# Optimization experiments

Hardware: AMD Instinct MI355X
Metric: run time of the kernel (lower is better)

## Reference

```python
import jax, jax.numpy as jnp
import numpy as np

INPUT = 28
STEPS = 28
HIDDEN = 128
LABELS = 10
FORGET_BIAS = 1.0


def setup_inputs() -> dict:
    key = jax.random.key(0)
    ks = jax.random.split(key, 4)
    B = 32768
    x = jax.random.normal(ks[0], (B, STEPS, INPUT), dtype=jnp.float32)
    # BasicLSTMCell kernel: [input+hidden, 4*hidden], gate order i, j, f, o
    W_lstm = jax.random.normal(ks[1], (INPUT + HIDDEN, 4 * HIDDEN), dtype=jnp.float32) * 0.08
    b_lstm = jnp.zeros((4 * HIDDEN,), dtype=jnp.float32)
    W_fc = jax.random.normal(ks[2], (HIDDEN, LABELS), dtype=jnp.float32) * 0.08
    b_fc = jnp.zeros((LABELS,), dtype=jnp.float32)
    return {"x": x, "W_lstm": W_lstm, "b_lstm": b_lstm, "W_fc": W_fc, "b_fc": b_fc}


def _lstm_step(carry, x_t, W, b):
    c, h = carry
    gates = jnp.concatenate([x_t, h], axis=-1) @ W + b  # [B, 4H]
    i, j, f, o = jnp.split(gates, 4, axis=-1)
    new_c = c * jax.nn.sigmoid(f + FORGET_BIAS) + jax.nn.sigmoid(i) * jnp.tanh(j)
    new_h = jnp.tanh(new_c) * jax.nn.sigmoid(o)
    return (new_c, new_h), None


def reference(x, W_lstm, b_lstm, W_fc, b_fc):
    B = x.shape[0]
    c0 = jnp.zeros((B, HIDDEN), dtype=x.dtype)
    h0 = jnp.zeros((B, HIDDEN), dtype=x.dtype)
    xs = jnp.swapaxes(x, 0, 1)  # [T, B, INPUT]
    (c, h), _ = jax.lax.scan(lambda carry, xt: _lstm_step(carry, xt, W_lstm, b_lstm), (c0, h0), xs)
    return h @ W_fc + b_fc  # logits [B, LABELS]
```

## Files before the change

### kernel.cpp

```cpp
#include <hip/hip_runtime.h>


typedef _Float16 f16x8 __attribute__((ext_vector_type(8)));
typedef float f32x4 __attribute__((ext_vector_type(4)));

#define HSTRIDE 136
#define L2E 1.44269504f

__global__ __launch_bounds__(512, 2)
void lstm_r13(const float* __restrict__ x,
              const float* __restrict__ W,
              const float* __restrict__ b,
              const float* __restrict__ Wfc,
              const float* __restrict__ bfc,
              float* __restrict__ out)
{
    __shared__ __align__(16) _Float16 h_s[2][128 * HSTRIDE];
    __shared__ __align__(16) _Float16 xs[2][8 * 512];

    const int tid  = threadIdx.x;
    const int wave = tid >> 6;
    const int lane = tid & 63;
    const int m16  = lane & 15;
    const int quad = lane >> 4;
    const int rbase = blockIdx.x * 128;
    const int hc = wave * 16 + m16;

    for (int i = tid; i < 128 * HSTRIDE; i += 512) h_s[0][i] = (_Float16)0.0f;
    for (int i = tid; i < 2 * 8 * 512; i += 512) ((_Float16*)xs)[i] = (_Float16)0.0f;

    f16x8 Wx[4];
    f16x8 Wh[4][4];
    float bias[4];
    #pragma unroll
    for (int g = 0; g < 4; g++) {
        const int col = g * 128 + wave * 16 + m16;
        const float sc = (g == 1) ? 2.0f * L2E : -L2E;
        bias[g] = sc * (b[col] + (g == 2 ? 1.0f : 0.0f));
        f16x8 w8;
        #pragma unroll
        for (int j = 0; j < 8; j++) {
            int kk = quad * 8 + j;
            w8[j] = (kk < 28) ? (_Float16)(sc * W[kk * 512 + col]) : (_Float16)0.0f;
        }
        Wx[g] = w8;
        #pragma unroll
        for (int ks = 0; ks < 4; ks++) {
            f16x8 h8;
            #pragma unroll
            for (int j = 0; j < 8; j++)
                h8[j] = (_Float16)(sc * W[(28 + ks * 32 + quad * 8 + j) * 512 + col]);
            Wh[ks][g] = h8;
        }
    }

    __syncthreads();

    int lsoff[7], goff[7];
    #pragma unroll
    for (int e = 0; e < 7; e++) {
        const int idx = e * 512 + tid;
        const int srow = idx / 28, sk = idx % 28;
        lsoff[e] = (srow >> 4) * 512 + (sk >> 3) * 128 + (srow & 15) * 8 + (sk & 7);
        goff[e]  = (rbase + srow) * 784 + sk;
    }

    #pragma unroll
    for (int e = 0; e < 7; e++) xs[0][lsoff[e]] = (_Float16)x[goff[e]];
    __syncthreads();

    float creg[32];
    #pragma unroll
    for (int i = 0; i < 32; i++) creg[i] = 0.0f;

    const int foff = quad * 128 + m16 * 8;

    int buf = 0;
    for (int t = 0; t < 28; t++) {
        const int nb = buf ^ 1;

        float xv[7];
        if (t < 27) {
            const float* xt = x + (t + 1) * 28;
            #pragma unroll
            for (int e = 0; e < 7; e++) xv[e] = xt[goff[e]];
        }

        f32x4 acc[2][4];

        {
            f16x8 ax = *(const f16x8*)(&xs[buf][foff]);
            #pragma unroll
            for (int g = 0; g < 4; g++) {
                acc[0][g] = (f32x4){bias[g], bias[g], bias[g], bias[g]};
                acc[0][g] = __builtin_amdgcn_mfma_f32_16x16x32_f16(ax, Wx[g], acc[0][g], 0, 0, 0);
            }
            #pragma unroll
            for (int ks = 0; ks < 4; ks++) {
                f16x8 ah = *(const f16x8*)(&h_s[buf][m16 * HSTRIDE + ks * 32 + quad * 8]);
                #pragma unroll
                for (int g = 0; g < 4; g++)
                    acc[0][g] = __builtin_amdgcn_mfma_f32_16x16x32_f16(ah, Wh[ks][g], acc[0][g], 0, 0, 0);
            }
        }

        #pragma unroll
        for (int mt = 0; mt < 8; mt++) {
            const int cur = mt & 1, nxt = cur ^ 1;

            if (mt < 7) {
                f16x8 axn = *(const f16x8*)(&xs[buf][(mt + 1) * 512 + foff]);
                #pragma unroll
                for (int g = 0; g < 4; g++) {
                    acc[nxt][g] = (f32x4){bias[g], bias[g], bias[g], bias[g]};
                    acc[nxt][g] = __builtin_amdgcn_mfma_f32_16x16x32_f16(axn, Wx[g], acc[nxt][g], 0, 0, 0);
                }
                #pragma unroll
                for (int ks = 0; ks < 4; ks++) {
                    f16x8 ahn = *(const f16x8*)(&h_s[buf][((mt + 1) * 16 + m16) * HSTRIDE + ks * 32 + quad * 8]);
                    #pragma unroll
                    for (int g = 0; g < 4; g++)
                        acc[nxt][g] = __builtin_amdgcn_mfma_f32_16x16x32_f16(ahn, Wh[ks][g], acc[nxt][g], 0, 0, 0);
                }
            }

            #pragma unroll
            for (int r = 0; r < 4; r++) {
                float ei  = __builtin_amdgcn_exp2f(acc[cur][0][r]);
                float e2j = __builtin_amdgcn_exp2f(acc[cur][1][r]);
                float ef  = __builtin_amdgcn_exp2f(acc[cur][2][r]);
                float eo  = __builtin_amdgcn_exp2f(acc[cur][3][r]);
                float A   = 1.0f + ei;
                float Bv  = e2j + 1.0f;
                float C   = 1.0f + ef;
                float AB  = A * Bv;
                float rP  = __builtin_amdgcn_rcpf(AB * C);
                float num = __builtin_fmaf(e2j, 2.0f * L2E, -2.0f * L2E);
                float cn  = __builtin_fmaf(creg[mt * 4 + r], AB * rP, num * (C * rP));
                creg[mt * 4 + r] = cn;
                float e2c = __builtin_amdgcn_exp2f(cn);
                float rQ  = __builtin_amdgcn_rcpf((e2c + 1.0f) * (1.0f + eo));
                float hv  = (e2c - 1.0f) * rQ;
                h_s[nb][(mt * 16 + quad * 4 + r) * HSTRIDE + hc] = (_Float16)hv;
            }
        }

        if (t < 27) {
            #pragma unroll
            for (int e = 0; e < 7; e++) xs[nb][lsoff[e]] = (_Float16)xv[e];
        }
        __syncthreads();
        buf = nb;
    }

    for (int i = tid; i < 1280; i += 512) {
        const int row = i / 10, lab = i % 10;
        float acc = bfc[lab];
        #pragma unroll 8
        for (int k = 0; k < 128; k++)
            acc += (float)h_s[buf][row * HSTRIDE + k] * Wfc[k * 10 + lab];
        out[(size_t)(rbase + row) * 10 + lab] = acc;
    }
}

extern "C" void kernel_launch(void* const* d_in, const int* in_sizes, int n_in,
                              void* d_out, int out_size, void* d_ws, size_t ws_size,
                              hipStream_t stream) {
    const float* x   = (const float*)d_in[0];
    const float* W   = (const float*)d_in[1];
    const float* b   = (const float*)d_in[2];
    const float* Wfc = (const float*)d_in[3];
    const float* bfc = (const float*)d_in[4];
    float* out = (float*)d_out;

    const int B = in_sizes[0] / (28 * 28);
    const int blocks = B / 128;
    lstm_r13<<<blocks, 512, 0, stream>>>(x, W, b, Wfc, bfc, out);
}
```

Before: 301.3 us.

## Halve rows per block, move input weights to LDS, raise occupancy to 4 blocks

Each block now handles 64 batch rows instead of 128, which doubles the grid and shrinks the cell-state registers. The input-projection weight fragments move from registers into shared memory, and the software-pipelined double accumulator is dropped, so launch bounds can request 4 blocks per CU. The aim is more waves in flight to hide the per-step sync and latency of the recurrence. The cost is extra LDS reads per tile, the loss of MFMA/activation overlap within a wave, and per-block weight setup repeated over twice as many blocks.

Measured after the change: 751.0 us. 149% more time.

```diff
diff --git a/kernel.cpp b/kernel.cpp
--- a/kernel.cpp
+++ b/kernel.cpp
@@ -7,34 +7,34 @@
 #define HSTRIDE 136
 #define L2E 1.44269504f
 
-__global__ __launch_bounds__(512, 2)
-void lstm_r13(const float* __restrict__ x,
+__global__ __launch_bounds__(512, 4)
+void lstm_r14(const float* __restrict__ x,
               const float* __restrict__ W,
               const float* __restrict__ b,
               const float* __restrict__ Wfc,
               const float* __restrict__ bfc,
               float* __restrict__ out)
 {
-    __shared__ __align__(16) _Float16 h_s[2][128 * HSTRIDE];
-    __shared__ __align__(16) _Float16 xs[2][8 * 512];
+    __shared__ __align__(16) _Float16 h_s[2][64 * HSTRIDE];
+    __shared__ __align__(16) _Float16 xs[2][4 * 512];
+    __shared__ __align__(16) _Float16 wx_s[8][4][64][8];
 
     const int tid  = threadIdx.x;
     const int wave = tid >> 6;
     const int lane = tid & 63;
     const int m16  = lane & 15;
     const int quad = lane >> 4;
-    const int rbase = blockIdx.x * 128;
+    const int rbase = blockIdx.x * 64;
     const int hc = wave * 16 + m16;
 
-    for (int i = tid; i < 128 * HSTRIDE; i += 512) h_s[0][i] = (_Float16)0.0f;
-    for (int i = tid; i < 2 * 8 * 512; i += 512) ((_Float16*)xs)[i] = (_Float16)0.0f;
+    for (int i = tid; i < 64 * HSTRIDE; i += 512) h_s[0][i] = (_Float16)0.0f;
+    for (int i = tid; i < 2 * 4 * 512; i += 512) ((_Float16*)xs)[i] = (_Float16)0.0f;
 
-    f16x8 Wx[4];
     f16x8 Wh[4][4];
     float bias[4];
     #pragma unroll
     for (int g = 0; g < 4; g++) {
-        const int col = g * 128 + wave * 16 + m16;
+        const int col = g * 128 + hc;
         const float sc = (g == 1) ? 2.0f * L2E : -L2E;
         bias[g] = sc * (b[col] + (g == 2 ? 1.0f : 0.0f));
         f16x8 w8;
@@ -43,7 +43,7 @@
             int kk = quad * 8 + j;
             w8[j] = (kk < 28) ? (_Float16)(sc * W[kk * 512 + col]) : (_Float16)0.0f;
         }
-        Wx[g] = w8;
+        *(f16x8*)&wx_s[wave][g][lane][0] = w8;
         #pragma unroll
         for (int ks = 0; ks < 4; ks++) {
             f16x8 h8;
@@ -56,80 +56,64 @@
 
     __syncthreads();
 
-    int lsoff[7], goff[7];
+    int lsoff[4], goff[4];
     #pragma unroll
-    for (int e = 0; e < 7; e++) {
+    for (int e = 0; e < 4; e++) {
         const int idx = e * 512 + tid;
         const int srow = idx / 28, sk = idx % 28;
         lsoff[e] = (srow >> 4) * 512 + (sk >> 3) * 128 + (srow & 15) * 8 + (sk & 7);
         goff[e]  = (rbase + srow) * 784 + sk;
     }
+    const bool e3ok = tid < 256;
 
     #pragma unroll
-    for (int e = 0; e < 7; e++) xs[0][lsoff[e]] = (_Float16)x[goff[e]];
+    for (int e = 0; e < 4; e++)
+        if (e < 3 || e3ok) xs[0][lsoff[e]] = (_Float16)x[goff[e]];
     __syncthreads();
 
-    float creg[32];
+    float creg[16];
     #pragma unroll
-    for (int i = 0; i < 32; i++) creg[i] = 0.0f;
+    for (int i = 0; i < 16; i++) creg[i] = 0.0f;
 
     const int foff = quad * 128 + m16 * 8;
+    const _Float16* wxp = &wx_s[wave][0][lane][0];
 
     int buf = 0;
     for (int t = 0; t < 28; t++) {
         const int nb = buf ^ 1;
 
-        float xv[7];
+        float xv[4];
         if (t < 27) {
             const float* xt = x + (t + 1) * 28;
             #pragma unroll
-            for (int e = 0; e < 7; e++) xv[e] = xt[goff[e]];
+            for (int e = 0; e < 4; e++)
+                if (e < 3 || e3ok) xv[e] = xt[goff[e]];
         }
 
-        f32x4 acc[2][4];
-
-        {
-            f16x8 ax = *(const f16x8*)(&xs[buf][foff]);
+        #pragma unroll
+        for (int mt = 0; mt < 4; mt++) {
+            f32x4 acc[4];
+            f16x8 ax = *(const f16x8*)(&xs[buf][mt * 512 + foff]);
             #pragma unroll
             for (int g = 0; g < 4; g++) {
-                acc[0][g] = (f32x4){bias[g], bias[g], bias[g], bias[g]};
-                acc[0][g] = __builtin_amdgcn_mfma_f32_16x16x32_f16(ax, Wx[g], acc[0][g], 0, 0, 0);
+                f16x8 wx = *(const f16x8*)(wxp + g * 512);
+                acc[g] = (f32x4){bias[g], bias[g], bias[g], bias[g]};
+                acc[g] = __builtin_amdgcn_mfma_f32_16x16x32_f16(ax, wx, acc[g], 0, 0, 0);
             }
             #pragma unroll
             for (int ks = 0; ks < 4; ks++) {
-                f16x8 ah = *(const f16x8*)(&h_s[buf][m16 * HSTRIDE + ks * 32 + quad * 8]);
+                f16x8 ah = *(const f16x8*)(&h_s[buf][(mt * 16 + m16) * HSTRIDE + ks * 32 + quad * 8]);
                 #pragma unroll
                 for (int g = 0; g < 4; g++)
-                    acc[0][g] = __builtin_amdgcn_mfma_f32_16x16x32_f16(ah, Wh[ks][g], acc[0][g], 0, 0, 0);
-            }
-        }
-
-        #pragma unroll
-        for (int mt = 0; mt < 8; mt++) {
-            const int cur = mt & 1, nxt = cur ^ 1;
-
-            if (mt < 7) {
-                f16x8 axn = *(const f16x8*)(&xs[buf][(mt + 1) * 512 + foff]);
-                #pragma unroll
-                for (int g = 0; g < 4; g++) {
-                    acc[nxt][g] = (f32x4){bias[g], bias[g], bias[g], bias[g]};
-                    acc[nxt][g] = __builtin_amdgcn_mfma_f32_16x16x32_f16(axn, Wx[g], acc[nxt][g], 0, 0, 0);
-                }
-                #pragma unroll
-                for (int ks = 0; ks < 4; ks++) {
-                    f16x8 ahn = *(const f16x8*)(&h_s[buf][((mt + 1) * 16 + m16) * HSTRIDE + ks * 32 + quad * 8]);
-                    #pragma unroll
-                    for (int g = 0; g < 4; g++)
-                        acc[nxt][g] = __builtin_amdgcn_mfma_f32_16x16x32_f16(ahn, Wh[ks][g], acc[nxt][g], 0, 0, 0);
-                }
+                    acc[g] = __builtin_amdgcn_mfma_f32_16x16x32_f16(ah, Wh[ks][g], acc[g], 0, 0, 0);
             }
 
             #pragma unroll
             for (int r = 0; r < 4; r++) {
-                float ei  = __builtin_amdgcn_exp2f(acc[cur][0][r]);
-                float e2j = __builtin_amdgcn_exp2f(acc[cur][1][r]);
-                float ef  = __builtin_amdgcn_exp2f(acc[cur][2][r]);
-                float eo  = __builtin_amdgcn_exp2f(acc[cur][3][r]);
+                float ei  = __builtin_amdgcn_exp2f(acc[0][r]);
+                float e2j = __builtin_amdgcn_exp2f(acc[1][r]);
+                float ef  = __builtin_amdgcn_exp2f(acc[2][r]);
+                float eo  = __builtin_amdgcn_exp2f(acc[3][r]);
                 float A   = 1.0f + ei;
                 float Bv  = e2j + 1.0f;
                 float C   = 1.0f + ef;
@@ -147,13 +131,14 @@
 
         if (t < 27) {
             #pragma unroll
-            for (int e = 0; e < 7; e++) xs[nb][lsoff[e]] = (_Float16)xv[e];
+            for (int e = 0; e < 4; e++)
+                if (e < 3 || e3ok) xs[nb][lsoff[e]] = (_Float16)xv[e];
         }
         __syncthreads();
         buf = nb;
     }
 
-    for (int i = tid; i < 1280; i += 512) {
+    for (int i = tid; i < 640; i += 512) {
         const int row = i / 10, lab = i % 10;
         float acc = bfc[lab];
         #pragma unroll 8
@@ -174,6 +159,6 @@
     float* out = (float*)d_out;
 
     const int B = in_sizes[0] / (28 * 28);
-    const int blocks = B / 128;
-    lstm_r13<<<blocks, 512, 0, stream>>>(x, W, b, Wfc, bfc, out);
+    const int blocks = B / 64;
+    lstm_r14<<<blocks, 512, 0, stream>>>(x, W, b, Wfc, bfc, out);
 }
```

## Fold bias into padded x MFMA slot, simplify x staging, add MFMA/VALU interleave schedule

Applied to the files above, without the earlier changes.

Puts the gate bias into the unused K padding of the input MFMA, as a split hi/lo fp16 pair multiplied by constant-one x slots, so accumulators start from zero instead of broadcast bias registers. Replaces the per-element div/mod x staging offsets with a direct 8-row strided mapping in which only threads with valid k load. Adds sched_group_barrier hints that interleave MFMA with VALU ops in the gate loop. These aim to cut register pressure and address arithmetic and to improve overlap, at the cost of relying on compiler scheduling hints and a slightly different rounding of the bias.

Result: slower. 314.0 us (+4.2%).

```diff
diff --git a/kernel.cpp b/kernel.cpp
--- a/kernel.cpp
+++ b/kernel.cpp
@@ -8,7 +8,7 @@
 #define L2E 1.44269504f
 
 __global__ __launch_bounds__(512, 2)
-void lstm_r13(const float* __restrict__ x,
+void lstm_r17(const float* __restrict__ x,
               const float* __restrict__ W,
               const float* __restrict__ b,
               const float* __restrict__ Wfc,
@@ -27,21 +27,29 @@
     const int hc = wave * 16 + m16;
 
     for (int i = tid; i < 128 * HSTRIDE; i += 512) h_s[0][i] = (_Float16)0.0f;
-    for (int i = tid; i < 2 * 8 * 512; i += 512) ((_Float16*)xs)[i] = (_Float16)0.0f;
+    for (int i = tid; i < 2 * 8 * 512; i += 512) {
+        const int q = i & 511;
+        const bool bslot = ((q >> 7) == 3) && (((q & 7) == 4) || ((q & 7) == 5));
+        ((_Float16*)xs)[i] = bslot ? (_Float16)1.0f : (_Float16)0.0f;
+    }
 
     f16x8 Wx[4];
     f16x8 Wh[4][4];
-    float bias[4];
     #pragma unroll
     for (int g = 0; g < 4; g++) {
-        const int col = g * 128 + wave * 16 + m16;
+        const int col = g * 128 + hc;
         const float sc = (g == 1) ? 2.0f * L2E : -L2E;
-        bias[g] = sc * (b[col] + (g == 2 ? 1.0f : 0.0f));
         f16x8 w8;
         #pragma unroll
         for (int j = 0; j < 8; j++) {
-            int kk = quad * 8 + j;
+            const int kk = quad * 8 + j;
             w8[j] = (kk < 28) ? (_Float16)(sc * W[kk * 512 + col]) : (_Float16)0.0f;
+        }
+        if (quad == 3) {
+            const float bv = sc * (b[col] + (g == 2 ? 1.0f : 0.0f));
+            const _Float16 hi = (_Float16)bv;
+            w8[4] = hi;
+            w8[5] = (_Float16)(bv - (float)hi);
         }
         Wx[g] = w8;
         #pragma unroll
@@ -56,17 +64,14 @@
 
     __syncthreads();
 
-    int lsoff[7], goff[7];
-    #pragma unroll
-    for (int e = 0; e < 7; e++) {
-        const int idx = e * 512 + tid;
-        const int srow = idx / 28, sk = idx % 28;
-        lsoff[e] = (srow >> 4) * 512 + (sk >> 3) * 128 + (srow & 15) * 8 + (sk & 7);
-        goff[e]  = (rbase + srow) * 784 + sk;
-    }
+    const int row16 = (tid >> 3) & 15;
+    const int sk    = ((tid >> 7) & 3) * 8 + (tid & 7);
+    const bool valid = (sk < 28);
+    const int goff0 = (rbase + row16) * 784 + sk;
 
     #pragma unroll
-    for (int e = 0; e < 7; e++) xs[0][lsoff[e]] = (_Float16)x[goff[e]];
+    for (int e = 0; e < 8; e++)
+        if (valid) xs[0][e * 512 + tid] = (_Float16)x[goff0 + e * 12544];
     __syncthreads();
 
     float creg[32];
@@ -74,16 +79,17 @@
     for (int i = 0; i < 32; i++) creg[i] = 0.0f;
 
     const int foff = quad * 128 + m16 * 8;
+    const f32x4 ZERO = (f32x4){0.0f, 0.0f, 0.0f, 0.0f};
 
     int buf = 0;
     for (int t = 0; t < 28; t++) {
         const int nb = buf ^ 1;
 
-        float xv[7];
-        if (t < 27) {
+        float xv[8];
+        if (t < 27 && valid) {
             const float* xt = x + (t + 1) * 28;
             #pragma unroll
-            for (int e = 0; e < 7; e++) xv[e] = xt[goff[e]];
+            for (int e = 0; e < 8; e++) xv[e] = xt[goff0 + e * 12544];
         }
 
         f32x4 acc[2][4];
@@ -91,10 +97,8 @@
         {
             f16x8 ax = *(const f16x8*)(&xs[buf][foff]);
             #pragma unroll
-            for (int g = 0; g < 4; g++) {
-                acc[0][g] = (f32x4){bias[g], bias[g], bias[g], bias[g]};
-                acc[0][g] = __builtin_amdgcn_mfma_f32_16x16x32_f16(ax, Wx[g], acc[0][g], 0, 0, 0);
-            }
+            for (int g = 0; g < 4; g++)
+                acc[0][g] = __builtin_amdgcn_mfma_f32_16x16x32_f16(ax, Wx[g], ZERO, 0, 0, 0);
             #pragma unroll
             for (int ks = 0; ks < 4; ks++) {
                 f16x8 ah = *(const f16x8*)(&h_s[buf][m16 * HSTRIDE + ks * 32 + quad * 8]);
@@ -111,10 +115,8 @@
             if (mt < 7) {
                 f16x8 axn = *(const f16x8*)(&xs[buf][(mt + 1) * 512 + foff]);
                 #pragma unroll
-                for (int g = 0; g < 4; g++) {
-                    acc[nxt][g] = (f32x4){bias[g], bias[g], bias[g], bias[g]};
-                    acc[nxt][g] = __builtin_amdgcn_mfma_f32_16x16x32_f16(axn, Wx[g], acc[nxt][g], 0, 0, 0);
-                }
+                for (int g = 0; g < 4; g++)
+                    acc[nxt][g] = __builtin_amdgcn_mfma_f32_16x16x32_f16(axn, Wx[g], ZERO, 0, 0, 0);
                 #pragma unroll
                 for (int ks = 0; ks < 4; ks++) {
                     f16x8 ahn = *(const f16x8*)(&h_s[buf][((mt + 1) * 16 + m16) * HSTRIDE + ks * 32 + quad * 8]);
@@ -143,11 +145,20 @@
                 float hv  = (e2c - 1.0f) * rQ;
                 h_s[nb][(mt * 16 + quad * 4 + r) * HSTRIDE + hc] = (_Float16)hv;
             }
+
+            __builtin_amdgcn_sched_group_barrier(0x100, 5, 0);
+            #pragma unroll
+            for (int rep = 0; rep < 20; rep++) {
+                __builtin_amdgcn_sched_group_barrier(0x008, 1, 0);
+                __builtin_amdgcn_sched_group_barrier(0x002, 5, 0);
+            }
+            __builtin_amdgcn_sched_group_barrier(0x200, 4, 0);
         }
 
-        if (t < 27) {
+        if (t < 27 && valid) {
             #pragma unroll
-            for (int e = 0; e < 7; e++) xs[nb][lsoff[e]] = (_Float16)xv[e];
+            for (int e = 0; e < 8; e++)
+                xs[nb][e * 512 + tid] = (_Float16)xv[e];
         }
         __syncthreads();
         buf = nb;
@@ -175,5 +186,5 @@
 
     const int B = in_sizes[0] / (28 * 28);
     const int blocks = B / 128;
-    lstm_r13<<<blocks, 512, 0, stream>>>(x, W, b, Wfc, bfc, out);
+    lstm_r17<<<blocks, 512, 0, stream>>>(x, W, b, Wfc, bfc, out);
 }
```
